# Kernel tuning notes

Hardware: AMD Instinct MI355X
Metric: run time of the kernel (lower is better)

Reference implementation:

```python
import jax, jax.numpy as jnp
import numpy as np

HEADS = 8
DIM_HEAD = 80
BATCH_SIZE = 2  # cfg batch (module init kwarg)


def setup_inputs() -> dict:
    key = jax.random.key(0)
    ks = jax.random.split(key, 6)
    F, S, D = 16, 1024, 640  # frames*batch, latent HW, query_dim
    hidden_states = jax.random.normal(ks[0], (F, S, D), jnp.float32)
    Wq = jax.random.normal(ks[1], (D, D), jnp.float32) * 0.02
    Wk = jax.random.normal(ks[2], (D, D), jnp.float32) * 0.02
    Wv = jax.random.normal(ks[3], (D, D), jnp.float32) * 0.02
    Wo = jax.random.normal(ks[4], (D, D), jnp.float32) * 0.02
    bo = jax.random.normal(ks[5], (D,), jnp.float32) * 0.02
    return {"hidden_states": hidden_states, "Wq": Wq, "Wk": Wk, "Wv": Wv, "Wo": Wo, "bo": bo}


def reference(hidden_states, Wq, Wk, Wv, Wo, bo):
    F, S, D = hidden_states.shape
    h, d = HEADS, DIM_HEAD
    scale = d ** -0.5

    q = hidden_states @ Wq  # [F, S, D]
    k = hidden_states @ Wk
    v = hidden_states @ Wv

    # cross-frame trick: replace every frame's K/V with the FIRST frame of its batch group
    vl = 1 if F < BATCH_SIZE else F // BATCH_SIZE  # video_length
    g = F // vl  # batch groups
    k = jnp.broadcast_to(k.reshape(g, vl, S, D)[:, :1], (g, vl, S, D)).reshape(F, S, D)
    v = jnp.broadcast_to(v.reshape(g, vl, S, D)[:, :1], (g, vl, S, D)).reshape(F, S, D)

    def to_heads(t):  # [F, S, h*d] -> [F*h, S, d]
        return t.reshape(F, S, h, d).transpose(0, 2, 1, 3).reshape(F * h, S, d)

    qh, kh, vh = to_heads(q), to_heads(k), to_heads(v)

    scores = jnp.einsum('bid,bjd->bij', qh, kh) * scale  # [F*h, S, S]
    probs = jax.nn.softmax(scores, axis=-1)
    out = jnp.einsum('bij,bjd->bid', probs, vh)  # [F*h, S, d]

    out = out.reshape(F, h, S, d).transpose(0, 2, 1, 3).reshape(F, S, h * d)
    return out @ Wo + bo
```

## Files before the change

kernel.cpp:

```cpp
#include <hip/hip_runtime.h>
#include <hip/hip_bf16.h>

typedef unsigned short u16;
typedef unsigned int u32;
typedef __attribute__((ext_vector_type(8))) short bf16x8;
typedef __attribute__((ext_vector_type(4))) float f32x4;

#define D640 640

__device__ __forceinline__ float b2f(u16 u) {
  union { u32 i; float f; } x; x.i = ((u32)u) << 16; return x.f;
}
__device__ __forceinline__ u16 f2b(float f) {
  union { __hip_bfloat16 h; u16 u; } c; c.h = __float2bfloat16(f); return c.u;
}
__device__ __forceinline__ u32 pack2(float a, float b) {
  union { __hip_bfloat162 h; u32 u; } c;
  c.h.x = __float2bfloat16(a); c.h.y = __float2bfloat16(b); return c.u;
}
__device__ __forceinline__ bf16x8 pack8(f32x4 lo, f32x4 hi) {
  bf16x8 r;
  r[0] = (short)f2b(lo[0]); r[1] = (short)f2b(lo[1]);
  r[2] = (short)f2b(lo[2]); r[3] = (short)f2b(lo[3]);
  r[4] = (short)f2b(hi[0]); r[5] = (short)f2b(hi[1]);
  r[6] = (short)f2b(hi[2]); r[7] = (short)f2b(hi[3]);
  return r;
}
__device__ __forceinline__ void gld_lds16(const u16* g, u16* l) {
  __builtin_amdgcn_global_load_lds((const __attribute__((address_space(1))) u32*)g,
                                   (__attribute__((address_space(3))) u32*)l, 16, 0, 0);
}

__global__ void detect_dtype(const u16* __restrict__ hs, u32* __restrict__ flag) {
  __shared__ u32 cnt;
  if (threadIdx.x == 0) cnt = 0;
  __syncthreads();
  int plaus = 0;
#pragma unroll
  for (int i = 0; i < 16; ++i) {
    u16 u = hs[(threadIdx.x * 16 + i) * 2];
    u32 e = (u >> 7) & 0xFF;
    if ((e >= 0x70 && e <= 0x8F) || (u & 0x7FFF) == 0) plaus++;
  }
  atomicAdd(&cnt, (u32)plaus);
  __syncthreads();
  if (threadIdx.x == 0) *flag = (cnt < 2048) ? 1u : 0u;
}

__global__ __launch_bounds__(256) void conv_hs(
    const void* __restrict__ hs, u16* __restrict__ out, const u32* __restrict__ flag)
{
  const size_t i = ((size_t)blockIdx.x * 256 + threadIdx.x) * 8;
  if (*flag) {
    const float* s = (const float*)hs;
    *(bf16x8*)(out + i) = pack8(*(const f32x4*)(s + i), *(const f32x4*)(s + i + 4));
  } else {
    *(bf16x8*)(out + i) = *(const bf16x8*)((const u16*)hs + i);
  }
}

__global__ __launch_bounds__(256) void transpose_w(
    const void* __restrict__ w0, const void* __restrict__ w1,
    const void* __restrict__ w2, const void* __restrict__ w3,
    u16* __restrict__ out, const u32* __restrict__ flag)
{
  __shared__ u16 t[32][33];
  const bool isF32 = (*flag != 0);
  const void* src = blockIdx.z == 0 ? w0 : blockIdx.z == 1 ? w1 : blockIdx.z == 2 ? w2 : w3;
  u16* dst = out + (size_t)blockIdx.z * 409600;
  int tx = threadIdx.x, ty = threadIdx.y;
  int x = blockIdx.x * 32 + tx;
  int y = blockIdx.y * 32 + ty;
  if (isF32) {
    const float* s = (const float*)src;
#pragma unroll
    for (int j = 0; j < 32; j += 8) t[ty + j][tx] = f2b(s[(y + j) * D640 + x]);
  } else {
    const u16* s = (const u16*)src;
#pragma unroll
    for (int j = 0; j < 32; j += 8) t[ty + j][tx] = s[(y + j) * D640 + x];
  }
  __syncthreads();
  int x2 = blockIdx.y * 32 + tx;
  int y2 = blockIdx.x * 32 + ty;
#pragma unroll
  for (int j = 0; j < 32; j += 8) dst[(y2 + j) * D640 + x2] = t[tx][ty + j];
}

__device__ __forceinline__ void gemm3_body(
    const u16* __restrict__ A, const u16* __restrict__ BT, void* __restrict__ Cv,
    float scale, const void* __restrict__ bias, bool isF32,
    int aRow0, int cMode, int bx, int by)
{
  __shared__ __align__(16) u16 Asub[128 * 32];
  __shared__ __align__(16) u16 Bsub[128 * 32];
  const bool cF32 = (cMode == 1) && isF32;
  const int tid = threadIdx.x;
  const int lane = tid & 63, w = tid >> 6;
  const int wr = w >> 1, wc = w & 1;
  const int l15 = lane & 15, g = lane >> 4;
  const int rowBase = bx * 128;
  const int colBase = by * 128;

  const int c0 = w * 128 + lane, c1 = c0 + 64;
  const u16* Ag0 = A + (size_t)(aRow0 + rowBase + (c0 >> 2)) * D640 + ((c0 & 3) ^ ((c0 >> 3) & 3)) * 8;
  const u16* Ag1 = A + (size_t)(aRow0 + rowBase + (c1 >> 2)) * D640 + ((c1 & 3) ^ ((c1 >> 3) & 3)) * 8;
  const u16* Bg0 = BT + (size_t)(colBase + (c0 >> 2)) * D640 + ((c0 & 3) ^ ((c0 >> 3) & 3)) * 8;
  const u16* Bg1 = BT + (size_t)(colBase + (c1 >> 2)) * D640 + ((c1 & 3) ^ ((c1 >> 3) & 3)) * 8;
  u16* lA0 = &Asub[w * 1024];
  u16* lA1 = &Asub[w * 1024 + 512];
  u16* lB0 = &Bsub[w * 1024];
  u16* lB1 = &Bsub[w * 1024 + 512];

  int aoff[4], boff[4];
#pragma unroll
  for (int f = 0; f < 4; ++f) {
    int R = wr * 64 + f * 16 + l15;
    aoff[f] = (R * 4 + (g ^ ((R >> 1) & 3))) * 8;
    int Cc = wc * 64 + f * 16 + l15;
    boff[f] = (Cc * 4 + (g ^ ((Cc >> 1) & 3))) * 8;
  }

  f32x4 acc[4][4];
#pragma unroll
  for (int i = 0; i < 4; ++i)
#pragma unroll
    for (int j = 0; j < 4; ++j) acc[i][j] = (f32x4){0.f, 0.f, 0.f, 0.f};

  for (int kt = 0; kt < 20; ++kt) {
    __syncthreads();
    gld_lds16(Ag0 + kt * 32, lA0);
    gld_lds16(Ag1 + kt * 32, lA1);
    gld_lds16(Bg0 + kt * 32, lB0);
    gld_lds16(Bg1 + kt * 32, lB1);
    __syncthreads();
    bf16x8 a[4], b[4];
#pragma unroll
    for (int f = 0; f < 4; ++f) a[f] = *(const bf16x8*)&Asub[aoff[f]];
#pragma unroll
    for (int f = 0; f < 4; ++f) b[f] = *(const bf16x8*)&Bsub[boff[f]];
    __builtin_amdgcn_s_setprio(1);
#pragma unroll
    for (int i = 0; i < 4; ++i)
#pragma unroll
      for (int j = 0; j < 4; ++j)
        acc[i][j] = __builtin_amdgcn_mfma_f32_16x16x32_bf16(a[i], b[j], acc[i][j], 0, 0, 0);
    __builtin_amdgcn_s_setprio(0);
  }

#pragma unroll
  for (int j = 0; j < 4; ++j) {
    int col = colBase + wc * 64 + j * 16 + l15;
    float bb = 0.f;
    if (bias) bb = cF32 ? ((const float*)bias)[col] : b2f(((const u16*)bias)[col]);
#pragma unroll
    for (int i = 0; i < 4; ++i) {
      int row = rowBase + wr * 64 + i * 16 + g * 4;
#pragma unroll
      for (int r = 0; r < 4; ++r) {
        float v = acc[i][j][r] * scale + bb;
        if (cMode == 2) {
          int rw = row + r;
          int rl = rw & 63;
          int slot = (rl & 32) | ((rl & 12) << 1) | (((rl >> 4) & 1) << 2) | (rl & 3);
          ((u16*)Cv)[(size_t)col * 1024 + (rw & ~63) + slot] = f2b(v);
        } else if (cF32) {
          ((float*)Cv)[(size_t)(row + r) * D640 + col] = v;
        } else {
          ((u16*)Cv)[(size_t)(row + r) * D640 + col] = f2b(v);
        }
      }
    }
  }
}

__global__ __launch_bounds__(256) void gemm3(
    const u16* __restrict__ A, const u16* __restrict__ BT, void* __restrict__ Cv,
    float scale, const void* __restrict__ bias, const u32* __restrict__ flag,
    int aRow0, int cMode)
{
  gemm3_body(A, BT, Cv, scale, bias, (*flag != 0), aRow0, cMode, blockIdx.x, blockIdx.y);
}

__global__ __launch_bounds__(256) void gemm_kv(
    const u16* __restrict__ hsb, const u16* __restrict__ WTk, const u16* __restrict__ WTv,
    u16* __restrict__ Kb, u16* __restrict__ Vb)
{
  const int z = blockIdx.z;
  const bool isK = (z < 2);
  const int grp = z & 1;
  const u16* bt = isK ? WTk : WTv;
  void* cv = isK ? (void*)(Kb + (size_t)grp * 1024 * 640)
                 : (void*)(Vb + (size_t)grp * 655360);
  gemm3_body(hsb, bt, cv, 1.f, nullptr, false, grp * 8192, isK ? 0 : 2,
             blockIdx.x, blockIdx.y);
}

__global__ __launch_bounds__(256, 3) void attn_kernel(
    const u16* __restrict__ Q, const u16* __restrict__ K2,
    const u16* __restrict__ VT, u16* __restrict__ AO)
{
  __shared__ __align__(16) u16 Klds[64 * 104];
  __shared__ __align__(16) u16 Vlds[80 * 72];

  const int tid = threadIdx.x, lane = tid & 63, w = tid >> 6;
  const int l15 = lane & 15, g = lane >> 4;
  const int qc = blockIdx.x, bh = blockIdx.y;
  const int f = bh >> 3, h = bh & 7;
  const int grp = f >> 3;

  const u16* Qp = Q + (size_t)(f * 1024 + qc * 128 + w * 32) * D640 + h * 80;
  const u16* Kp = K2 + (size_t)(grp * 1024) * D640 + h * 80;
  const u16* Vp = VT + (size_t)(grp * 8 + h) * 80 * 1024;

  if (tid < 128) {
    const bf16x8 z8 = {0, 0, 0, 0, 0, 0, 0, 0};
    *(bf16x8*)&Klds[(tid >> 1) * 104 + 80 + (tid & 1) * 8] = z8;
  }

  bf16x8 qreg[2][3];
#pragma unroll
  for (int qb = 0; qb < 2; ++qb)
#pragma unroll
    for (int dc = 0; dc < 3; ++dc) {
      int dd = dc * 32 + g * 8;
      if (dd < 80) qreg[qb][dc] = *(const bf16x8*)(Qp + (l15 + 16 * qb) * D640 + dd);
      else         qreg[qb][dc] = (bf16x8){0, 0, 0, 0, 0, 0, 0, 0};
    }

  f32x4 acc[2][5];
#pragma unroll
  for (int qb = 0; qb < 2; ++qb)
#pragma unroll
    for (int db = 0; db < 5; ++db) acc[qb][db] = (f32x4){0.f, 0.f, 0.f, 0.f};
  float mreg[2] = {0.f, 0.f};
  float lrow[2] = {0.f, 0.f};

  const u16* gsrc[5];
  u16* ldst[5];
  int step[5];
#pragma unroll
  for (int i = 0; i < 5; ++i) {
    int c = tid + i * 256;
    if (c < 640) {
      int row = c / 10, cc = c - row * 10;
      gsrc[i] = Kp + row * D640 + cc * 8;
      ldst[i] = &Klds[row * 104 + cc * 8];
      step[i] = 64 * D640;
    } else {
      int c2 = c - 640, d = c2 >> 3, cc = c2 & 7;
      gsrc[i] = Vp + d * 1024 + cc * 8;
      ldst[i] = &Vlds[d * 72 + cc * 8];
      step[i] = 64;
    }
  }

  bf16x8 pre[5];
#pragma unroll
  for (int i = 0; i < 5; ++i) pre[i] = *(const bf16x8*)gsrc[i];

  for (int it = 0; it < 16; ++it) {
    __syncthreads();
#pragma unroll
    for (int i = 0; i < 5; ++i) *(bf16x8*)ldst[i] = pre[i];
    __syncthreads();
    if (it < 15) {
#pragma unroll
      for (int i = 0; i < 5; ++i) pre[i] = *(const bf16x8*)(gsrc[i] + (it + 1) * step[i]);
    }

    f32x4 st[4][2];
#pragma unroll
    for (int kb = 0; kb < 4; ++kb)
#pragma unroll
      for (int qb = 0; qb < 2; ++qb) st[kb][qb] = (f32x4){0.f, 0.f, 0.f, 0.f};
    __builtin_amdgcn_s_setprio(1);
#pragma unroll
    for (int dc = 0; dc < 3; ++dc)
#pragma unroll
      for (int kb = 0; kb < 4; ++kb) {
        bf16x8 ka = *(const bf16x8*)&Klds[(kb * 16 + l15) * 104 + dc * 32 + g * 8];
        st[kb][0] = __builtin_amdgcn_mfma_f32_16x16x32_bf16(ka, qreg[0][dc], st[kb][0], 0, 0, 0);
        st[kb][1] = __builtin_amdgcn_mfma_f32_16x16x32_bf16(ka, qreg[1][dc], st[kb][1], 0, 0, 0);
      }
    __builtin_amdgcn_s_setprio(0);

    float mt[2];
#pragma unroll
    for (int qb = 0; qb < 2; ++qb) {
      float m01 = fmaxf(fmaxf(st[0][qb][0], st[0][qb][1]), fmaxf(st[0][qb][2], st[0][qb][3]));
      float m23 = fmaxf(fmaxf(st[1][qb][0], st[1][qb][1]), fmaxf(st[1][qb][2], st[1][qb][3]));
      float m45 = fmaxf(fmaxf(st[2][qb][0], st[2][qb][1]), fmaxf(st[2][qb][2], st[2][qb][3]));
      float m67 = fmaxf(fmaxf(st[3][qb][0], st[3][qb][1]), fmaxf(st[3][qb][2], st[3][qb][3]));
      mt[qb] = fmaxf(fmaxf(m01, m23), fmaxf(m45, m67));
    }

    if (__any((mt[0] > mreg[0] + 8.f) || (mt[1] > mreg[1] + 8.f))) {
#pragma unroll
      for (int qb = 0; qb < 2; ++qb) {
        float m = mt[qb];
        m = fmaxf(m, __shfl_xor(m, 16, 64));
        m = fmaxf(m, __shfl_xor(m, 32, 64));
        float mn = fmaxf(mreg[qb], m);
        float scl = exp2f(mreg[qb] - mn);
        mreg[qb] = mn;
        lrow[qb] *= scl;
        float s_[4];
#pragma unroll
        for (int r = 0; r < 4; ++r)
          s_[r] = __shfl(scl, (lane & 48) | (g * 4 + r), 64);
#pragma unroll
        for (int db = 0; db < 5; ++db)
#pragma unroll
          for (int r = 0; r < 4; ++r) acc[qb][db][r] *= s_[r];
      }
    }

    bf16x8 pa[2][2];
#pragma unroll
    for (int qb = 0; qb < 2; ++qb) {
      float sum = 0.f;
      u32 wlo[4], whi[4];
#pragma unroll
      for (int kb = 0; kb < 4; ++kb) {
        float p0 = exp2f(st[kb][qb][0] - mreg[qb]);
        float p1 = exp2f(st[kb][qb][1] - mreg[qb]);
        float p2 = exp2f(st[kb][qb][2] - mreg[qb]);
        float p3 = exp2f(st[kb][qb][3] - mreg[qb]);
        sum += (p0 + p1) + (p2 + p3);
        wlo[kb] = pack2(p0, p1);
        whi[kb] = pack2(p2, p3);
      }
      lrow[qb] += sum;
#pragma unroll
      for (int kc = 0; kc < 2; ++kc) {
        union { u32 u[4]; bf16x8 v; } cvt;
        cvt.u[0] = wlo[2 * kc];
        cvt.u[1] = whi[2 * kc];
        cvt.u[2] = wlo[2 * kc + 1];
        cvt.u[3] = whi[2 * kc + 1];
        pa[qb][kc] = cvt.v;
      }
    }

    __builtin_amdgcn_s_setprio(1);
#pragma unroll
    for (int kc = 0; kc < 2; ++kc) {
#pragma unroll
      for (int db = 0; db < 5; ++db) {
        bf16x8 bv = *(const bf16x8*)&Vlds[(db * 16 + l15) * 72 + kc * 32 + g * 8];
        acc[0][db] = __builtin_amdgcn_mfma_f32_16x16x32_bf16(pa[0][kc], bv, acc[0][db], 0, 0, 0);
        acc[1][db] = __builtin_amdgcn_mfma_f32_16x16x32_bf16(pa[1][kc], bv, acc[1][db], 0, 0, 0);
      }
    }
    __builtin_amdgcn_s_setprio(0);
  }

  u16* Op = AO + (size_t)(f * 1024 + qc * 128 + w * 32) * D640 + h * 80;
#pragma unroll
  for (int qb = 0; qb < 2; ++qb) {
    float lr = lrow[qb];
    lr += __shfl_xor(lr, 16, 64);
    lr += __shfl_xor(lr, 32, 64);
    float i_[4];
#pragma unroll
    for (int r = 0; r < 4; ++r)
      i_[r] = 1.f / __shfl(lr, (lane & 48) | (g * 4 + r), 64);
#pragma unroll
    for (int db = 0; db < 5; ++db)
#pragma unroll
      for (int r = 0; r < 4; ++r)
        Op[(qb * 16 + g * 4 + r) * D640 + db * 16 + l15] = f2b(acc[qb][db][r] * i_[r]);
  }
}

extern "C" void kernel_launch(void* const* d_in, const int* in_sizes, int n_in,
                              void* d_out, int out_size, void* d_ws, size_t ws_size,
                              hipStream_t stream) {
  (void)in_sizes; (void)n_in; (void)out_size; (void)ws_size;
  const void* hs = d_in[0];
  const void* wq = d_in[1];
  const void* wk = d_in[2];
  const void* wv = d_in[3];
  const void* wo = d_in[4];
  const void* bo = d_in[5];
  u16* ws = (u16*)d_ws;

  u16* WT  = ws;
  u16* Qb  = ws + 1638400;
  u16* Kb  = Qb + 10485760;
  u16* Vb  = Kb + 1310720;
  u16* hsb = Vb + 1310720;
  u16* AOb = hsb;
  u32* flag = (u32*)(hsb + 10485760);

  const float QSCALE = 0.11180339887498949f * 1.44269504088896340f;

  detect_dtype<<<1, 256, 0, stream>>>((const u16*)hs, flag);
  conv_hs<<<5120, 256, 0, stream>>>(hs, hsb, flag);
  transpose_w<<<dim3(20, 20, 4), dim3(32, 8), 0, stream>>>(wq, wk, wv, wo, WT, flag);

  gemm3<<<dim3(128, 5), 256, 0, stream>>>(hsb, WT, Qb, QSCALE, nullptr, flag, 0, 0);
  gemm_kv<<<dim3(8, 5, 4), 256, 0, stream>>>(hsb, WT + 409600, WT + 819200, Kb, Vb);

  attn_kernel<<<dim3(8, 128), 256, 0, stream>>>(Qb, Kb, Vb, AOb);

  gemm3<<<dim3(128, 5), 256, 0, stream>>>(AOb, WT + 1228800, d_out, 1.f, bo, flag, 0, 1);
}
```

Before: 165.7 us.

## Fuse hidden-state conversion and Q/K/V projections into one GEMM kernel

Removes the separate fp32-to-bf16 conversion pass and instead converts the hidden states in registers while loading A tiles inside a new combined QKV GEMM. The Q and K/V projection launches become one 640-block grid with 128x160 tiles, which cuts a launch and avoids writing and re-reading a bf16 copy of the activations. In exchange, A is now staged through registers with plain stores instead of async global-to-LDS loads, fp32 A reads double the read bandwidth per tile, and the wider tile uses more accumulators.

```diff
diff --git a/kernel.cpp b/kernel.cpp
--- a/kernel.cpp
+++ b/kernel.cpp
@@ -45,18 +45,6 @@
   atomicAdd(&cnt, (u32)plaus);
   __syncthreads();
   if (threadIdx.x == 0) *flag = (cnt < 2048) ? 1u : 0u;
-}
-
-__global__ __launch_bounds__(256) void conv_hs(
-    const void* __restrict__ hs, u16* __restrict__ out, const u32* __restrict__ flag)
-{
-  const size_t i = ((size_t)blockIdx.x * 256 + threadIdx.x) * 8;
-  if (*flag) {
-    const float* s = (const float*)hs;
-    *(bf16x8*)(out + i) = pack8(*(const f32x4*)(s + i), *(const f32x4*)(s + i + 4));
-  } else {
-    *(bf16x8*)(out + i) = *(const bf16x8*)((const u16*)hs + i);
-  }
 }
 
 __global__ __launch_bounds__(256) void transpose_w(
@@ -87,20 +75,157 @@
   for (int j = 0; j < 32; j += 8) dst[(y2 + j) * D640 + x2] = t[tx][ty + j];
 }
 
-__device__ __forceinline__ void gemm3_body(
+__global__ __launch_bounds__(256) void gemm_qkv(
+    const void* __restrict__ hsv, const u16* __restrict__ WT,
+    u16* __restrict__ Qb, u16* __restrict__ Kb, u16* __restrict__ Vb,
+    const u32* __restrict__ flag, float qscale)
+{
+  __shared__ __align__(16) u16 Asub[128 * 32];
+  __shared__ __align__(16) u16 Bsub[160 * 32];
+  const bool aF32 = (*flag != 0);
+  const int tid = threadIdx.x;
+  const int lane = tid & 63, w = tid >> 6;
+  const int wr = w >> 1, wc = w & 1;
+  const int l15 = lane & 15, g = lane >> 4;
+
+  const int bid = blockIdx.x;
+  int bx, by, aRow0, cMode;
+  const u16* BT;
+  u16* Cv;
+  float scale;
+  if (bid < 512) {
+    bx = bid >> 2; by = bid & 3; aRow0 = 0; cMode = 0;
+    BT = WT; Cv = Qb; scale = qscale;
+  } else {
+    const int t = bid - 512;
+    const bool isK = (t < 64);
+    const int t2 = t & 63;
+    const int grp = t2 >> 5;
+    bx = (t2 >> 2) & 7; by = t2 & 3; aRow0 = grp * 8192;
+    cMode = isK ? 0 : 2;
+    BT = isK ? (WT + 409600) : (WT + 819200);
+    Cv = isK ? (Kb + (size_t)grp * 655360) : (Vb + (size_t)grp * 655360);
+    scale = 1.f;
+  }
+  const int rowBase = bx * 128;
+  const int colBase = by * 160;
+
+  const int ar0 = tid >> 2, ar1 = ar0 + 64, gc = tid & 3;
+  const int als0 = ar0 * 4 + (gc ^ ((ar0 >> 1) & 3));
+  const int als1 = ar1 * 4 + (gc ^ ((ar1 >> 1) & 3));
+  const size_t aIdx0 = (size_t)(aRow0 + rowBase + ar0) * D640 + gc * 8;
+  const size_t aIdx1 = (size_t)(aRow0 + rowBase + ar1) * D640 + gc * 8;
+
+  const int bc0 = w * 64 + lane;
+  const int bc1 = bc0 + 256;
+  const int bc2 = 512 + w * 64 + lane;
+  const u16* Bg0 = BT + (size_t)(colBase + (bc0 >> 2)) * D640 + ((bc0 & 3) ^ ((bc0 >> 3) & 3)) * 8;
+  const u16* Bg1 = BT + (size_t)(colBase + (bc1 >> 2)) * D640 + ((bc1 & 3) ^ ((bc1 >> 3) & 3)) * 8;
+  const u16* Bg2 = BT + (size_t)(colBase + ((bc2 >> 2) & 255)) * D640 + ((bc2 & 3) ^ ((bc2 >> 3) & 3)) * 8;
+  u16* lB0 = &Bsub[(size_t)w * 64 * 8];
+  u16* lB1 = &Bsub[((size_t)w * 64 + 256) * 8];
+  u16* lB2 = &Bsub[((size_t)w * 64 + 512) * 8];
+
+  int aoff[4], boff[5];
+#pragma unroll
+  for (int f = 0; f < 4; ++f) {
+    int R = wr * 64 + f * 16 + l15;
+    aoff[f] = (R * 4 + (g ^ ((R >> 1) & 3))) * 8;
+  }
+#pragma unroll
+  for (int j = 0; j < 5; ++j) {
+    int Cc = wc * 80 + j * 16 + l15;
+    boff[j] = (Cc * 4 + (g ^ ((Cc >> 1) & 3))) * 8;
+  }
+
+  f32x4 acc[4][5];
+#pragma unroll
+  for (int i = 0; i < 4; ++i)
+#pragma unroll
+    for (int j = 0; j < 5; ++j) acc[i][j] = (f32x4){0.f, 0.f, 0.f, 0.f};
+
+  bf16x8 ra0, ra1;
+  if (aF32) {
+    const float* Af = (const float*)hsv;
+    ra0 = pack8(*(const f32x4*)(Af + aIdx0), *(const f32x4*)(Af + aIdx0 + 4));
+    ra1 = pack8(*(const f32x4*)(Af + aIdx1), *(const f32x4*)(Af + aIdx1 + 4));
+  } else {
+    const u16* Ab = (const u16*)hsv;
+    ra0 = *(const bf16x8*)(Ab + aIdx0);
+    ra1 = *(const bf16x8*)(Ab + aIdx1);
+  }
+
+  for (int kt = 0; kt < 20; ++kt) {
+    __syncthreads();
+    *(bf16x8*)&Asub[als0 * 8] = ra0;
+    *(bf16x8*)&Asub[als1 * 8] = ra1;
+    gld_lds16(Bg0 + kt * 32, lB0);
+    gld_lds16(Bg1 + kt * 32, lB1);
+    if (w < 2) gld_lds16(Bg2 + kt * 32, lB2);
+    __syncthreads();
+    if (kt < 19) {
+      const int k1 = (kt + 1) * 32;
+      if (aF32) {
+        const float* Af = (const float*)hsv;
+        ra0 = pack8(*(const f32x4*)(Af + aIdx0 + k1), *(const f32x4*)(Af + aIdx0 + k1 + 4));
+        ra1 = pack8(*(const f32x4*)(Af + aIdx1 + k1), *(const f32x4*)(Af + aIdx1 + k1 + 4));
+      } else {
+        const u16* Ab = (const u16*)hsv;
+        ra0 = *(const bf16x8*)(Ab + aIdx0 + k1);
+        ra1 = *(const bf16x8*)(Ab + aIdx1 + k1);
+      }
+    }
+    bf16x8 a[4], b[5];
+#pragma unroll
+    for (int f = 0; f < 4; ++f) a[f] = *(const bf16x8*)&Asub[aoff[f]];
+#pragma unroll
+    for (int j = 0; j < 5; ++j) b[j] = *(const bf16x8*)&Bsub[boff[j]];
+    __builtin_amdgcn_s_setprio(1);
+#pragma unroll
+    for (int i = 0; i < 4; ++i)
+#pragma unroll
+      for (int j = 0; j < 5; ++j)
+        acc[i][j] = __builtin_amdgcn_mfma_f32_16x16x32_bf16(a[i], b[j], acc[i][j], 0, 0, 0);
+    __builtin_amdgcn_s_setprio(0);
+  }
+
+#pragma unroll
+  for (int j = 0; j < 5; ++j) {
+    int col = colBase + wc * 80 + j * 16 + l15;
+#pragma unroll
+    for (int i = 0; i < 4; ++i) {
+      int row = rowBase + wr * 64 + i * 16 + g * 4;
+#pragma unroll
+      for (int r = 0; r < 4; ++r) {
+        float v = acc[i][j][r] * scale;
+        if (cMode == 2) {
+          int rw = row + r;
+          int rl = rw & 63;
+          int slot = (rl & 32) | ((rl & 12) << 1) | (((rl >> 4) & 1) << 2) | (rl & 3);
+          ((u16*)Cv)[(size_t)col * 1024 + (rw & ~63) + slot] = f2b(v);
+        } else {
+          ((u16*)Cv)[(size_t)(row + r) * D640 + col] = f2b(v);
+        }
+      }
+    }
+  }
+}
+
+__global__ __launch_bounds__(256) void gemm3(
     const u16* __restrict__ A, const u16* __restrict__ BT, void* __restrict__ Cv,
-    float scale, const void* __restrict__ bias, bool isF32,
-    int aRow0, int cMode, int bx, int by)
+    float scale, const void* __restrict__ bias, const u32* __restrict__ flag,
+    int aRow0, int cMode)
 {
   __shared__ __align__(16) u16 Asub[128 * 32];
   __shared__ __align__(16) u16 Bsub[128 * 32];
+  const bool isF32 = (*flag != 0);
   const bool cF32 = (cMode == 1) && isF32;
   const int tid = threadIdx.x;
   const int lane = tid & 63, w = tid >> 6;
   const int wr = w >> 1, wc = w & 1;
   const int l15 = lane & 15, g = lane >> 4;
-  const int rowBase = bx * 128;
-  const int colBase = by * 128;
+  const int rowBase = blockIdx.x * 128;
+  const int colBase = blockIdx.y * 128;
 
   const int c0 = w * 128 + lane, c1 = c0 + 64;
   const u16* Ag0 = A + (size_t)(aRow0 + rowBase + (c0 >> 2)) * D640 + ((c0 & 3) ^ ((c0 >> 3) & 3)) * 8;
@@ -159,41 +284,11 @@
 #pragma unroll
       for (int r = 0; r < 4; ++r) {
         float v = acc[i][j][r] * scale + bb;
-        if (cMode == 2) {
-          int rw = row + r;
-          int rl = rw & 63;
-          int slot = (rl & 32) | ((rl & 12) << 1) | (((rl >> 4) & 1) << 2) | (rl & 3);
-          ((u16*)Cv)[(size_t)col * 1024 + (rw & ~63) + slot] = f2b(v);
-        } else if (cF32) {
-          ((float*)Cv)[(size_t)(row + r) * D640 + col] = v;
-        } else {
-          ((u16*)Cv)[(size_t)(row + r) * D640 + col] = f2b(v);
-        }
-      }
-    }
-  }
-}
-
-__global__ __launch_bounds__(256) void gemm3(
-    const u16* __restrict__ A, const u16* __restrict__ BT, void* __restrict__ Cv,
-    float scale, const void* __restrict__ bias, const u32* __restrict__ flag,
-    int aRow0, int cMode)
-{
-  gemm3_body(A, BT, Cv, scale, bias, (*flag != 0), aRow0, cMode, blockIdx.x, blockIdx.y);
-}
-
-__global__ __launch_bounds__(256) void gemm_kv(
-    const u16* __restrict__ hsb, const u16* __restrict__ WTk, const u16* __restrict__ WTv,
-    u16* __restrict__ Kb, u16* __restrict__ Vb)
-{
-  const int z = blockIdx.z;
-  const bool isK = (z < 2);
-  const int grp = z & 1;
-  const u16* bt = isK ? WTk : WTv;
-  void* cv = isK ? (void*)(Kb + (size_t)grp * 1024 * 640)
-                 : (void*)(Vb + (size_t)grp * 655360);
-  gemm3_body(hsb, bt, cv, 1.f, nullptr, false, grp * 8192, isK ? 0 : 2,
-             blockIdx.x, blockIdx.y);
+        if (cF32) ((float*)Cv)[(size_t)(row + r) * D640 + col] = v;
+        else      ((u16*)Cv)[(size_t)(row + r) * D640 + col] = f2b(v);
+      }
+    }
+  }
 }
 
 __global__ __launch_bounds__(256, 3) void attn_kernel(
@@ -390,18 +485,15 @@
   u16* Qb  = ws + 1638400;
   u16* Kb  = Qb + 10485760;
   u16* Vb  = Kb + 1310720;
-  u16* hsb = Vb + 1310720;
-  u16* AOb = hsb;
-  u32* flag = (u32*)(hsb + 10485760);
+  u16* AOb = Vb + 1310720;
+  u32* flag = (u32*)(AOb + 10485760);
 
   const float QSCALE = 0.11180339887498949f * 1.44269504088896340f;
 
   detect_dtype<<<1, 256, 0, stream>>>((const u16*)hs, flag);
-  conv_hs<<<5120, 256, 0, stream>>>(hs, hsb, flag);
   transpose_w<<<dim3(20, 20, 4), dim3(32, 8), 0, stream>>>(wq, wk, wv, wo, WT, flag);
 
-  gemm3<<<dim3(128, 5), 256, 0, stream>>>(hsb, WT, Qb, QSCALE, nullptr, flag, 0, 0);
-  gemm_kv<<<dim3(8, 5, 4), 256, 0, stream>>>(hsb, WT + 409600, WT + 819200, Kb, Vb);
+  gemm_qkv<<<640, 256, 0, stream>>>(hs, WT, Qb, Kb, Vb, flag, QSCALE);
 
   attn_kernel<<<dim3(8, 128), 256, 0, stream>>>(Qb, Kb, Vb, AOb);
 
```

New measurement: 181.1 us. +9.3%, slower.
